# Kernel tuning notes

Hardware: AMD Instinct MI355X
Metric: run time of the kernel (lower is better)

The kernel has to match this reference:

```python
import jax, jax.numpy as jnp
import numpy as np

EPS_DIST = 1e-8
EPS_BN = 1e-5


def _bn_relu(x, g, b):
    # training-mode BatchNorm1d over (batch, spatial) per channel, then ReLU
    mean = jnp.mean(x, axis=(0, 2), keepdims=True)
    var = jnp.mean((x - mean) ** 2, axis=(0, 2), keepdims=True)
    xhat = (x - mean) * jax.lax.rsqrt(var + EPS_BN)
    return jax.nn.relu(xhat * g[None, :, None] + b[None, :, None])


def setup_inputs() -> dict:
    key = jax.random.key(0)
    ks = jax.random.split(key, 8)
    B, N, M, C1, C2 = 8, 16384, 4096, 64, 256
    return {
        "p1": jax.random.normal(ks[0], (B, N, 3), jnp.float32),
        "p2": jax.random.normal(ks[1], (B, M, 3), jnp.float32),
        "f1": jax.random.normal(ks[2], (B, C1, N), jnp.float32),
        "f2": jax.random.normal(ks[3], (B, C2, M), jnp.float32),
        "idx": jax.random.randint(ks[4], (B, N, 3), 0, M, jnp.int64),
        "W1": jax.random.normal(ks[5], (256, C1 + C2), jnp.float32) * 0.05,
        "g1": jnp.ones((256,), jnp.float32),
        "b1": jnp.zeros((256,), jnp.float32),
        "W2": jax.random.normal(ks[6], (256, 256), jnp.float32) * 0.05,
        "g2": jnp.ones((256,), jnp.float32),
        "b2": jnp.zeros((256,), jnp.float32),
    }


def reference(p1, p2, f1, f2, idx, W1, g1, b1, W2, g2, b2):
    B = p1.shape[0]
    b_ix = jnp.arange(B)[:, None, None]  # batch index for gathers
    # --- three_interpolation: inverse-squared-distance weighted 3-NN interp ---
    nbr_xyz = p2[b_ix, idx]                     # [B, N, 3, 3]
    d2 = jnp.sum((p1[:, :, None, :] - nbr_xyz) ** 2, axis=-1)  # [B, N, 3]
    recip = 1.0 / (d2 + EPS_DIST)
    weight = recip / jnp.sum(recip, axis=-1, keepdims=True)    # [B, N, 3]
    f2_nbr = jnp.swapaxes(f2, 1, 2)[b_ix, idx]  # [B, N, 3, C2]
    interp = jnp.einsum("bnkc,bnk->bcn", f2_nbr, weight)       # [B, C2, N]
    # --- concat + two 1x1 conv + BN + ReLU blocks ---
    x = jnp.concatenate((f1, interp), axis=1)   # [B, C1+C2, N]
    x = _bn_relu(jnp.einsum("oi,bin->bon", W1, x), g1, b1)
    x = _bn_relu(jnp.einsum("oi,bin->bon", W2, x), g2, b2)
    return x
```

## Files before the change

kernel.cpp:

```cpp
#include <hip/hip_runtime.h>
#include <hip/hip_bf16.h>

#define BB 8
#define NN 16384
#define MM 4096
#define C1 64
#define C2 256
#define K1 320
#define CO 256
#define MTOT (BB * NN)

#define STATS_OFF 0
#define FLAG_OFF  8192
#define W1B_OFF   16384
#define W2B_OFF   180224
#define F2T_OFF   327680
#define XT_OFF    (327680 + 16777216)
#define H2_OFF    (327680 + 16777216 + 83886080)

typedef short v8s __attribute__((ext_vector_type(8)));
typedef float v4f __attribute__((ext_vector_type(4)));

__device__ __forceinline__ float bf2f(unsigned short u) {
    unsigned v = ((unsigned)u) << 16;
    float f;
    __builtin_memcpy(&f, &v, 4);
    return f;
}
__device__ __forceinline__ unsigned short f2bf(float f) {
    unsigned u;
    __builtin_memcpy(&u, &f, 4);
    unsigned r = u + 0x7fffu + ((u >> 16) & 1u);
    return (unsigned short)(r >> 16);
}
__device__ __forceinline__ void gload16(const unsigned short* g, unsigned short* l) {
    __builtin_amdgcn_global_load_lds((const __attribute__((address_space(1))) unsigned int*)g,
                                     (__attribute__((address_space(3))) unsigned int*)l, 16, 0, 0);
}

__global__ void k_prep(const void* idx_raw, int* flag64, float* stats,
                       const float* __restrict__ W1, unsigned short* __restrict__ W1b,
                       const float* __restrict__ W2, unsigned short* __restrict__ W2b) {
    int blk = blockIdx.x;
    int t = threadIdx.x;
    if (blk < 320) {
        int e = blk * 256 + t;
        W1b[e] = f2bf(W1[e]);
    } else if (blk < 576) {
        int e = (blk - 320) * 256 + t;
        W2b[e] = f2bf(W2[e]);
    } else {
        for (int i = t; i < 8 * 256; i += 256) stats[i] = 0.f;
        if (t == 0) {
            const int* a = (const int*)idx_raw;
            int all0 = 1;
            for (int j = 1; j < 64; j += 2) all0 &= (a[j] == 0);
            *flag64 = all0;
        }
    }
}

__global__ void k_tr_f2(const float* __restrict__ f2, unsigned short* __restrict__ f2t) {
    __shared__ float tile[64][33];
    int b = blockIdx.z;
    int c0 = blockIdx.y * 64;
    int m0 = blockIdx.x * 32;
    int t = threadIdx.x;
    int lm = t & 31, lc = t >> 5;
    const float* src = f2 + ((size_t)b * C2 + c0) * MM + m0;
#pragma unroll
    for (int j = 0; j < 8; ++j)
        tile[lc + 8 * j][lm] = src[(size_t)(lc + 8 * j) * MM + lm];
    __syncthreads();
    int m = t >> 3, c8 = (t & 7) * 8;
    unsigned short tmp[8];
#pragma unroll
    for (int k = 0; k < 8; ++k) tmp[k] = f2bf(tile[c8 + k][m]);
    uint4 v;
    v.x = (unsigned)tmp[0] | ((unsigned)tmp[1] << 16);
    v.y = (unsigned)tmp[2] | ((unsigned)tmp[3] << 16);
    v.z = (unsigned)tmp[4] | ((unsigned)tmp[5] << 16);
    v.w = (unsigned)tmp[6] | ((unsigned)tmp[7] << 16);
    *(uint4*)&f2t[((size_t)b * MM + m0 + m) * C2 + c0 + c8] = v;
}

__global__ void k_tr_f1(const float* __restrict__ f1, unsigned short* __restrict__ xT) {
    __shared__ float tile[64][33];
    int b = blockIdx.z;
    int n0 = blockIdx.x * 32;
    int t = threadIdx.x;
    int lm = t & 31, lc = t >> 5;
    const float* src = f1 + ((size_t)b * C1) * NN + n0;
#pragma unroll
    for (int j = 0; j < 8; ++j)
        tile[lc + 8 * j][lm] = src[(size_t)(lc + 8 * j) * NN + lm];
    __syncthreads();
    int m = t >> 3, c8 = (t & 7) * 8;
    unsigned short tmp[8];
#pragma unroll
    for (int k = 0; k < 8; ++k) tmp[k] = f2bf(tile[c8 + k][m]);
    uint4 v;
    v.x = (unsigned)tmp[0] | ((unsigned)tmp[1] << 16);
    v.y = (unsigned)tmp[2] | ((unsigned)tmp[3] << 16);
    v.z = (unsigned)tmp[4] | ((unsigned)tmp[5] << 16);
    v.w = (unsigned)tmp[6] | ((unsigned)tmp[7] << 16);
    *(uint4*)&xT[((size_t)b * NN + n0 + m) * K1 + c8] = v;
}

__global__ void k_interp(const float* __restrict__ p1, const float* __restrict__ p2,
                         const void* __restrict__ idxv, const int* __restrict__ flag64,
                         const unsigned short* __restrict__ f2t,
                         unsigned short* __restrict__ xT) {
    int t = threadIdx.x;
    int p = t >> 5, lane = t & 31;
    size_t pt = (size_t)blockIdx.x * 8 + p;
    int b = (int)(pt >> 14);
    int m0, m1, m2;
    if (*flag64) {
        const long long* id = (const long long*)idxv;
        m0 = (int)id[pt * 3 + 0]; m1 = (int)id[pt * 3 + 1]; m2 = (int)id[pt * 3 + 2];
    } else {
        const int* id = (const int*)idxv;
        m0 = id[pt * 3 + 0]; m1 = id[pt * 3 + 1]; m2 = id[pt * 3 + 2];
    }
    float qx = p1[pt * 3 + 0], qy = p1[pt * 3 + 1], qz = p1[pt * 3 + 2];
    const float* pb = p2 + (size_t)b * MM * 3;
    float dx, dy, dz;
    dx = qx - pb[m0 * 3 + 0]; dy = qy - pb[m0 * 3 + 1]; dz = qz - pb[m0 * 3 + 2];
    float d0 = dx * dx + dy * dy + dz * dz;
    dx = qx - pb[m1 * 3 + 0]; dy = qy - pb[m1 * 3 + 1]; dz = qz - pb[m1 * 3 + 2];
    float d1 = dx * dx + dy * dy + dz * dz;
    dx = qx - pb[m2 * 3 + 0]; dy = qy - pb[m2 * 3 + 1]; dz = qz - pb[m2 * 3 + 2];
    float d2v = dx * dx + dy * dy + dz * dz;
    float r0 = 1.f / (d0 + 1e-8f), r1 = 1.f / (d1 + 1e-8f), r2 = 1.f / (d2v + 1e-8f);
    float inv = 1.f / (r0 + r1 + r2);
    float w0 = r0 * inv, w1 = r1 * inv, w2 = r2 * inv;

    const unsigned short* fb = f2t + (size_t)b * MM * C2;
    int c0 = lane * 8;
    uint4 va = *(const uint4*)(fb + (size_t)m0 * C2 + c0);
    uint4 vb = *(const uint4*)(fb + (size_t)m1 * C2 + c0);
    uint4 vc = *(const uint4*)(fb + (size_t)m2 * C2 + c0);

    float r[8];
    {
        const unsigned av[4] = {va.x, va.y, va.z, va.w};
        const unsigned bv[4] = {vb.x, vb.y, vb.z, vb.w};
        const unsigned cv[4] = {vc.x, vc.y, vc.z, vc.w};
#pragma unroll
        for (int q = 0; q < 4; ++q) {
            r[2 * q + 0] = w0 * bf2f((unsigned short)(av[q] & 0xffff))
                         + w1 * bf2f((unsigned short)(bv[q] & 0xffff))
                         + w2 * bf2f((unsigned short)(cv[q] & 0xffff));
            r[2 * q + 1] = w0 * bf2f((unsigned short)(av[q] >> 16))
                         + w1 * bf2f((unsigned short)(bv[q] >> 16))
                         + w2 * bf2f((unsigned short)(cv[q] >> 16));
        }
    }
    uint4 outv;
    outv.x = (unsigned)f2bf(r[0]) | ((unsigned)f2bf(r[1]) << 16);
    outv.y = (unsigned)f2bf(r[2]) | ((unsigned)f2bf(r[3]) << 16);
    outv.z = (unsigned)f2bf(r[4]) | ((unsigned)f2bf(r[5]) << 16);
    outv.w = (unsigned)f2bf(r[6]) | ((unsigned)f2bf(r[7]) << 16);
    *(uint4*)(xT + pt * K1 + C1 + c0) = outv;
}

#define TM 128
#define TN 128
#define TK 64
__launch_bounds__(256)
__global__ void k_gemm1(const unsigned short* __restrict__ xT,
                        const unsigned short* __restrict__ W1b,
                        unsigned short* __restrict__ h1,
                        float* __restrict__ sum1, float* __restrict__ ssq1) {
    __shared__ unsigned short smem[TM * TK + TN * TK];
    __shared__ float s_sum[TN], s_ssq[TN];
    unsigned short* As = smem;
    unsigned short* Bs = smem + TM * TK;
    const int t = threadIdx.x;
    const int lane = t & 63, w = t >> 6;
    const int wm = w >> 1, wc = w & 1;
    const long rbase = (long)blockIdx.x * TM;
    const int cb = blockIdx.y * TN;

    if (t < TN) { s_sum[t] = 0.f; s_ssq[t] = 0.f; }

    v4f acc[4][4];
#pragma unroll
    for (int r = 0; r < 4; ++r)
#pragma unroll
        for (int c = 0; c < 4; ++c) acc[r][c] = (v4f)(0.f);

    const int srow = w * 32 + (lane >> 3);
    const int sch = (lane & 7) * 8;
    const unsigned short* Ag = xT + (rbase + srow) * K1 + sch;
    const unsigned short* Bg = W1b + (size_t)(cb + srow) * K1 + sch;

    for (int k0 = 0; k0 < K1; k0 += TK) {
#pragma unroll
        for (int j = 0; j < 4; ++j) {
            gload16(Ag + (size_t)(j * 8) * K1 + k0, As + (w * 32 + j * 8) * TK);
            gload16(Bg + (size_t)(j * 8) * K1 + k0, Bs + (w * 32 + j * 8) * TK);
        }
        __syncthreads();
        const unsigned short* ApL = As + (wm * 64 + (lane & 15)) * TK + (lane >> 4) * 8;
        const unsigned short* BpL = Bs + (wc * 64 + (lane & 15)) * TK + (lane >> 4) * 8;
#pragma unroll
        for (int ks = 0; ks < 2; ++ks) {
            v8s af[4], bg[4];
#pragma unroll
            for (int r = 0; r < 4; ++r) af[r] = *(const v8s*)(ApL + r * 16 * TK + ks * 32);
#pragma unroll
            for (int c = 0; c < 4; ++c) bg[c] = *(const v8s*)(BpL + c * 16 * TK + ks * 32);
#pragma unroll
            for (int r = 0; r < 4; ++r)
#pragma unroll
                for (int c = 0; c < 4; ++c)
                    acc[r][c] = __builtin_amdgcn_mfma_f32_16x16x32_bf16(af[r], bg[c], acc[r][c], 0, 0, 0);
        }
        __syncthreads();
    }

    const int q = lane >> 4, ln = lane & 15;
#pragma unroll
    for (int c = 0; c < 4; ++c) {
        int col = wc * 64 + c * 16 + ln;
        int cc = col >> 3, ci = col & 7;
        float s = 0.f, sq = 0.f;
#pragma unroll
        for (int r = 0; r < 4; ++r)
#pragma unroll
            for (int i = 0; i < 4; ++i) {
                int row = wm * 64 + r * 16 + q * 4 + i;
                float v = acc[r][c][i];
                smem[row * 128 + 8 * (cc ^ (row & 15)) + ci] = f2bf(v);
                s += v; sq += v * v;
            }
        atomicAdd(&s_sum[col], s);
        atomicAdd(&s_ssq[col], sq);
    }
    __syncthreads();
    {
        int rr = t >> 4, cc2 = t & 15;
#pragma unroll
        for (int j = 0; j < 8; ++j) {
            int row = rr + 16 * j;
            uint4 v = *(const uint4*)&smem[row * 128 + 8 * (cc2 ^ (row & 15))];
            *(uint4*)&h1[(size_t)(rbase + row) * CO + cb + cc2 * 8] = v;
        }
    }
    if (t < TN) {
        atomicAdd(&sum1[cb + t], s_sum[t]);
        atomicAdd(&ssq1[cb + t], s_ssq[t]);
    }
}

__launch_bounds__(256)
__global__ void k_gemm2(const unsigned short* __restrict__ h1,
                        const unsigned short* __restrict__ W2b,
                        const float* __restrict__ sum1, const float* __restrict__ ssq1,
                        const float* __restrict__ g1, const float* __restrict__ b1,
                        unsigned short* __restrict__ h2,
                        float* __restrict__ sum2, float* __restrict__ ssq2) {
    __shared__ unsigned short smem[TM * TK + TN * TK];
    __shared__ float s_sum[TN], s_ssq[TN];
    __shared__ float sc1[CO], sh1[CO];
    unsigned short* As = smem;
    unsigned short* Bs = smem + TM * TK;
    const int t = threadIdx.x;
    const int lane = t & 63, w = t >> 6;
    const int wm = w >> 1, wc = w & 1;
    const long rbase = (long)blockIdx.x * TM;
    const int cb = blockIdx.y * TN;

    {
        const float invn = 1.f / (float)MTOT;
        float m = sum1[t] * invn;
        float v = ssq1[t] * invn - m * m;
        float s = g1[t] * rsqrtf(v + 1e-5f);
        sc1[t] = s;
        sh1[t] = b1[t] - m * s;
    }
    if (t < TN) { s_sum[t] = 0.f; s_ssq[t] = 0.f; }
    __syncthreads();

    v4f acc[4][4];
#pragma unroll
    for (int r = 0; r < 4; ++r)
#pragma unroll
        for (int c = 0; c < 4; ++c) acc[r][c] = (v4f)(0.f);

    const int srow = w * 32 + (lane >> 3);
    const int sch = (lane & 7) * 8;
    const unsigned short* Ag = h1 + (rbase + srow) * CO + sch;
    const unsigned short* Bg = W2b + (size_t)(cb + srow) * CO + sch;
    unsigned short* AsW = As + srow * TK + sch;

    for (int k0 = 0; k0 < CO; k0 += TK) {
#pragma unroll
        for (int j = 0; j < 4; ++j)
            gload16(Bg + (size_t)(j * 8) * CO + k0, Bs + (w * 32 + j * 8) * TK);
        float4 sca = *(const float4*)(sc1 + k0 + sch);
        float4 scb = *(const float4*)(sc1 + k0 + sch + 4);
        float4 sha = *(const float4*)(sh1 + k0 + sch);
        float4 shb = *(const float4*)(sh1 + k0 + sch + 4);
#pragma unroll
        for (int j = 0; j < 4; ++j) {
            uint4 av = *(const uint4*)(Ag + (size_t)(j * 8) * CO + k0);
            float y0 = fmaxf(bf2f((unsigned short)(av.x & 0xffff)) * sca.x + sha.x, 0.f);
            float y1 = fmaxf(bf2f((unsigned short)(av.x >> 16)) * sca.y + sha.y, 0.f);
            float y2 = fmaxf(bf2f((unsigned short)(av.y & 0xffff)) * sca.z + sha.z, 0.f);
            float y3 = fmaxf(bf2f((unsigned short)(av.y >> 16)) * sca.w + sha.w, 0.f);
            float y4 = fmaxf(bf2f((unsigned short)(av.z & 0xffff)) * scb.x + shb.x, 0.f);
            float y5 = fmaxf(bf2f((unsigned short)(av.z >> 16)) * scb.y + shb.y, 0.f);
            float y6 = fmaxf(bf2f((unsigned short)(av.w & 0xffff)) * scb.z + shb.z, 0.f);
            float y7 = fmaxf(bf2f((unsigned short)(av.w >> 16)) * scb.w + shb.w, 0.f);
            uint4 ov;
            ov.x = (unsigned)f2bf(y0) | ((unsigned)f2bf(y1) << 16);
            ov.y = (unsigned)f2bf(y2) | ((unsigned)f2bf(y3) << 16);
            ov.z = (unsigned)f2bf(y4) | ((unsigned)f2bf(y5) << 16);
            ov.w = (unsigned)f2bf(y6) | ((unsigned)f2bf(y7) << 16);
            *(uint4*)(AsW + (j * 8) * TK) = ov;
        }
        __syncthreads();
        const unsigned short* ApL = As + (wm * 64 + (lane & 15)) * TK + (lane >> 4) * 8;
        const unsigned short* BpL = Bs + (wc * 64 + (lane & 15)) * TK + (lane >> 4) * 8;
#pragma unroll
        for (int ks = 0; ks < 2; ++ks) {
            v8s af[4], bg4[4];
#pragma unroll
            for (int r = 0; r < 4; ++r) af[r] = *(const v8s*)(ApL + r * 16 * TK + ks * 32);
#pragma unroll
            for (int c = 0; c < 4; ++c) bg4[c] = *(const v8s*)(BpL + c * 16 * TK + ks * 32);
#pragma unroll
            for (int r = 0; r < 4; ++r)
#pragma unroll
                for (int c = 0; c < 4; ++c)
                    acc[r][c] = __builtin_amdgcn_mfma_f32_16x16x32_bf16(af[r], bg4[c], acc[r][c], 0, 0, 0);
        }
        __syncthreads();
    }

    const int q = lane >> 4, ln = lane & 15;
    const int b = (int)(rbase >> 14);
    const int nb = (int)(rbase & (NN - 1));
#pragma unroll
    for (int c = 0; c < 4; ++c) {
        int ol = wc * 64 + c * 16 + ln;
        float s = 0.f, sq = 0.f;
#pragma unroll
        for (int r = 0; r < 4; ++r)
#pragma unroll
            for (int i = 0; i < 4; ++i) {
                int row = wm * 64 + r * 16 + q * 4 + i;
                int rc = row >> 3, ri = row & 7;
                float v = acc[r][c][i];
                smem[ol * 128 + 8 * (rc ^ (ol & 15)) + ri] = f2bf(v);
                s += v; sq += v * v;
            }
        atomicAdd(&s_sum[ol], s);
        atomicAdd(&s_ssq[ol], sq);
    }
    __syncthreads();
    {
        int oo = t >> 4, nc = t & 15;
#pragma unroll
        for (int j = 0; j < 8; ++j) {
            int ol = oo + 16 * j;
            uint4 v = *(const uint4*)&smem[ol * 128 + 8 * (nc ^ (ol & 15))];
            *(uint4*)&h2[(((size_t)(b * CO + cb + ol)) << 14) + nb + nc * 8] = v;
        }
    }
    if (t < TN) {
        atomicAdd(&sum2[cb + t], s_sum[t]);
        atomicAdd(&ssq2[cb + t], s_ssq[t]);
    }
}

__global__ void k_apply(const unsigned short* __restrict__ h2,
                        const float* __restrict__ sum2, const float* __restrict__ ssq2,
                        const float* __restrict__ g2, const float* __restrict__ b2,
                        float* __restrict__ out) {
    __shared__ float ss[2];
    int o = (blockIdx.x >> 4) & 255;
    if (threadIdx.x == 0) {
        const float invn = 1.f / (float)MTOT;
        float m = sum2[o] * invn;
        float v = ssq2[o] * invn - m * m;
        float s = g2[o] * rsqrtf(v + 1e-5f);
        ss[0] = s;
        ss[1] = b2[o] - m * s;
    }
    __syncthreads();
    float s = ss[0], d = ss[1];
    size_t i = ((size_t)blockIdx.x * 256 + threadIdx.x) * 4;
    ushort4 hv = *(const ushort4*)(h2 + i);
    float4 v;
    v.x = fmaxf(bf2f(hv.x) * s + d, 0.f);
    v.y = fmaxf(bf2f(hv.y) * s + d, 0.f);
    v.z = fmaxf(bf2f(hv.z) * s + d, 0.f);
    v.w = fmaxf(bf2f(hv.w) * s + d, 0.f);
    *(float4*)&out[i] = v;
}

extern "C" void kernel_launch(void* const* d_in, const int* in_sizes, int n_in,
                              void* d_out, int out_size, void* d_ws, size_t ws_size,
                              hipStream_t stream) {
    const float* p1 = (const float*)d_in[0];
    const float* p2 = (const float*)d_in[1];
    const float* f1 = (const float*)d_in[2];
    const float* f2 = (const float*)d_in[3];
    const void*  idx = d_in[4];
    const float* W1 = (const float*)d_in[5];
    const float* g1 = (const float*)d_in[6];
    const float* b1 = (const float*)d_in[7];
    const float* W2 = (const float*)d_in[8];
    const float* g2 = (const float*)d_in[9];
    const float* b2 = (const float*)d_in[10];
    float* out = (float*)d_out;

    char* ws = (char*)d_ws;
    float* stats = (float*)(ws + STATS_OFF);
    float* sum1 = stats + 0;     float* ssq1 = stats + 256;
    float* sum2 = stats + 1024;  float* ssq2 = stats + 1280;
    int* flag64 = (int*)(ws + FLAG_OFF);
    unsigned short* W1b = (unsigned short*)(ws + W1B_OFF);
    unsigned short* W2b = (unsigned short*)(ws + W2B_OFF);
    unsigned short* f2t = (unsigned short*)(ws + F2T_OFF);
    unsigned short* xT  = (unsigned short*)(ws + XT_OFF);
    unsigned short* h2  = (unsigned short*)(ws + H2_OFF);

    unsigned short* h1 = (unsigned short*)d_out;

    k_prep<<<577, 256, 0, stream>>>(idx, flag64, stats, W1, W1b, W2, W2b);
    k_tr_f2<<<dim3(MM / 32, C2 / 64, BB), 256, 0, stream>>>(f2, f2t);
    k_tr_f1<<<dim3(NN / 32, 1, BB), 256, 0, stream>>>(f1, xT);
    k_interp<<<MTOT / 8, 256, 0, stream>>>(p1, p2, idx, flag64, f2t, xT);
    k_gemm1<<<dim3(MTOT / TM, CO / TN), 256, 0, stream>>>(xT, W1b, h1, sum1, ssq1);
    k_gemm2<<<dim3(MTOT / TM, CO / TN), 256, 0, stream>>>(h1, W2b, sum1, ssq1, g1, b1, h2, sum2, ssq2);
    k_apply<<<(int)((size_t)out_size / 4 / 256), 256, 0, stream>>>(h2, sum2, ssq2, g2, b2, out);
}
```

Baseline: 425.1 us.

## Double-buffer LDS tiles, swizzle layout, and write GEMM epilogues directly

Both GEMM kernels now use two LDS buffers so the next K-tile's global loads (and, in gemm2, the next activation register prefetch) are issued before the current tile's MFMAs, with manual waitcnt and barriers replacing __syncthreads. LDS rows get an XOR swizzle on the 16-byte chunk index to reduce bank conflicts, and gemm1 swaps operand roles so outputs come out transposed. The epilogues drop the LDS staging and block-level shared atomics: each wave writes packed bf16 pairs straight to global memory and reduces BN statistics with lane shuffles before issuing global atomics. In exchange, LDS use doubles, which may lower occupancy. The direct stores are narrower, 8-byte writes, so coalescing may suffer.

```diff
diff --git a/kernel.cpp b/kernel.cpp
--- a/kernel.cpp
+++ b/kernel.cpp
@@ -173,18 +173,14 @@
                         const unsigned short* __restrict__ W1b,
                         unsigned short* __restrict__ h1,
                         float* __restrict__ sum1, float* __restrict__ ssq1) {
-    __shared__ unsigned short smem[TM * TK + TN * TK];
-    __shared__ float s_sum[TN], s_ssq[TN];
-    unsigned short* As = smem;
-    unsigned short* Bs = smem + TM * TK;
+    __shared__ unsigned short smem[2][TM * TK + TN * TK];
     const int t = threadIdx.x;
     const int lane = t & 63, w = t >> 6;
-    const int wm = w >> 1, wc = w & 1;
+    const int cosub = (w >> 1) * 64;
+    const int nsub = (w & 1) * 64;
     const long rbase = (long)blockIdx.x * TM;
     const int cb = blockIdx.y * TN;
 
-    if (t < TN) { s_sum[t] = 0.f; s_ssq[t] = 0.f; }
-
     v4f acc[4][4];
 #pragma unroll
     for (int r = 0; r < 4; ++r)
@@ -192,66 +188,90 @@
         for (int c = 0; c < 4; ++c) acc[r][c] = (v4f)(0.f);
 
     const int srow = w * 32 + (lane >> 3);
-    const int sch = (lane & 7) * 8;
+    const int sch = ((lane & 7) ^ ((lane >> 3) & 7)) * 8;
     const unsigned short* Ag = xT + (rbase + srow) * K1 + sch;
     const unsigned short* Bg = W1b + (size_t)(cb + srow) * K1 + sch;
 
+#pragma unroll
+    for (int j = 0; j < 4; ++j) {
+        gload16(Ag + (size_t)(j * 8) * K1, smem[0] + (w * 32 + j * 8) * TK);
+        gload16(Bg + (size_t)(j * 8) * K1, smem[0] + TM * TK + (w * 32 + j * 8) * TK);
+    }
+
+    const int ln = lane & 15, q = lane >> 4;
+    const int xr = (lane & 7) * 8;
+
+#pragma unroll
     for (int k0 = 0; k0 < K1; k0 += TK) {
-#pragma unroll
-        for (int j = 0; j < 4; ++j) {
-            gload16(Ag + (size_t)(j * 8) * K1 + k0, As + (w * 32 + j * 8) * TK);
-            gload16(Bg + (size_t)(j * 8) * K1 + k0, Bs + (w * 32 + j * 8) * TK);
-        }
-        __syncthreads();
-        const unsigned short* ApL = As + (wm * 64 + (lane & 15)) * TK + (lane >> 4) * 8;
-        const unsigned short* BpL = Bs + (wc * 64 + (lane & 15)) * TK + (lane >> 4) * 8;
+        const int p = (k0 >> 6) & 1;
+        if (k0 + TK < K1) {
+#pragma unroll
+            for (int j = 0; j < 4; ++j) {
+                gload16(Ag + (size_t)(j * 8) * K1 + k0 + TK, smem[p ^ 1] + (w * 32 + j * 8) * TK);
+                gload16(Bg + (size_t)(j * 8) * K1 + k0 + TK, smem[p ^ 1] + TM * TK + (w * 32 + j * 8) * TK);
+            }
+            asm volatile("s_waitcnt vmcnt(8)" ::: "memory");
+        } else {
+            asm volatile("s_waitcnt vmcnt(0)" ::: "memory");
+        }
+        asm volatile("s_barrier" ::: "memory");
+        const unsigned short* Xs = smem[p];
+        const unsigned short* Ws = smem[p] + TM * TK;
 #pragma unroll
         for (int ks = 0; ks < 2; ++ks) {
-            v8s af[4], bg[4];
-#pragma unroll
-            for (int r = 0; r < 4; ++r) af[r] = *(const v8s*)(ApL + r * 16 * TK + ks * 32);
-#pragma unroll
-            for (int c = 0; c < 4; ++c) bg[c] = *(const v8s*)(BpL + c * 16 * TK + ks * 32);
+            const int off = (q * 8 + ks * 32) ^ xr;
+            v8s af[4], bx[4];
+#pragma unroll
+            for (int r = 0; r < 4; ++r) af[r] = *(const v8s*)(Ws + (cosub + r * 16 + ln) * TK + off);
+#pragma unroll
+            for (int c = 0; c < 4; ++c) bx[c] = *(const v8s*)(Xs + (nsub + c * 16 + ln) * TK + off);
 #pragma unroll
             for (int r = 0; r < 4; ++r)
 #pragma unroll
                 for (int c = 0; c < 4; ++c)
-                    acc[r][c] = __builtin_amdgcn_mfma_f32_16x16x32_bf16(af[r], bg[c], acc[r][c], 0, 0, 0);
-        }
-        __syncthreads();
-    }
-
-    const int q = lane >> 4, ln = lane & 15;
-#pragma unroll
-    for (int c = 0; c < 4; ++c) {
-        int col = wc * 64 + c * 16 + ln;
-        int cc = col >> 3, ci = col & 7;
-        float s = 0.f, sq = 0.f;
+                    acc[r][c] = __builtin_amdgcn_mfma_f32_16x16x32_bf16(af[r], bx[c], acc[r][c], 0, 0, 0);
+        }
+        if (k0 + TK < K1) asm volatile("s_barrier" ::: "memory");
+    }
+
+    float s[4][4], sq[4][4];
+#pragma unroll
+    for (int r = 0; r < 4; ++r)
+#pragma unroll
+        for (int i = 0; i < 4; ++i) { s[r][i] = 0.f; sq[r][i] = 0.f; }
+#pragma unroll
+    for (int r = 0; r < 4; ++r) {
+#pragma unroll
+        for (int c = 0; c < 4; ++c) {
+            float v0 = acc[r][c][0], v1 = acc[r][c][1], v2 = acc[r][c][2], v3 = acc[r][c][3];
+            uint2 ov;
+            ov.x = (unsigned)f2bf(v0) | ((unsigned)f2bf(v1) << 16);
+            ov.y = (unsigned)f2bf(v2) | ((unsigned)f2bf(v3) << 16);
+            *(uint2*)&h1[(size_t)(rbase + nsub + c * 16 + ln) * CO + cb + cosub + r * 16 + q * 4] = ov;
+            s[r][0] += v0; sq[r][0] += v0 * v0;
+            s[r][1] += v1; sq[r][1] += v1 * v1;
+            s[r][2] += v2; sq[r][2] += v2 * v2;
+            s[r][3] += v3; sq[r][3] += v3 * v3;
+        }
+    }
+#pragma unroll
+    for (int m = 1; m <= 8; m <<= 1) {
 #pragma unroll
         for (int r = 0; r < 4; ++r)
 #pragma unroll
             for (int i = 0; i < 4; ++i) {
-                int row = wm * 64 + r * 16 + q * 4 + i;
-                float v = acc[r][c][i];
-                smem[row * 128 + 8 * (cc ^ (row & 15)) + ci] = f2bf(v);
-                s += v; sq += v * v;
+                s[r][i] += __shfl_xor(s[r][i], m);
+                sq[r][i] += __shfl_xor(sq[r][i], m);
             }
-        atomicAdd(&s_sum[col], s);
-        atomicAdd(&s_ssq[col], sq);
-    }
-    __syncthreads();
-    {
-        int rr = t >> 4, cc2 = t & 15;
-#pragma unroll
-        for (int j = 0; j < 8; ++j) {
-            int row = rr + 16 * j;
-            uint4 v = *(const uint4*)&smem[row * 128 + 8 * (cc2 ^ (row & 15))];
-            *(uint4*)&h1[(size_t)(rbase + row) * CO + cb + cc2 * 8] = v;
-        }
-    }
-    if (t < TN) {
-        atomicAdd(&sum1[cb + t], s_sum[t]);
-        atomicAdd(&ssq1[cb + t], s_ssq[t]);
+    }
+    if (ln == 0) {
+#pragma unroll
+        for (int r = 0; r < 4; ++r)
+#pragma unroll
+            for (int i = 0; i < 4; ++i) {
+                atomicAdd(&sum1[cb + cosub + r * 16 + q * 4 + i], s[r][i]);
+                atomicAdd(&ssq1[cb + cosub + r * 16 + q * 4 + i], sq[r][i]);
+            }
     }
 }
 
@@ -262,14 +282,12 @@
                         const float* __restrict__ g1, const float* __restrict__ b1,
                         unsigned short* __restrict__ h2,
                         float* __restrict__ sum2, float* __restrict__ ssq2) {
-    __shared__ unsigned short smem[TM * TK + TN * TK];
-    __shared__ float s_sum[TN], s_ssq[TN];
+    __shared__ unsigned short smem[2][TM * TK + TN * TK];
     __shared__ float sc1[CO], sh1[CO];
-    unsigned short* As = smem;
-    unsigned short* Bs = smem + TM * TK;
     const int t = threadIdx.x;
     const int lane = t & 63, w = t >> 6;
-    const int wm = w >> 1, wc = w & 1;
+    const int nsub = (w >> 1) * 64;
+    const int cosub = (w & 1) * 64;
     const long rbase = (long)blockIdx.x * TM;
     const int cb = blockIdx.y * TN;
 
@@ -277,11 +295,10 @@
         const float invn = 1.f / (float)MTOT;
         float m = sum1[t] * invn;
         float v = ssq1[t] * invn - m * m;
-        float s = g1[t] * rsqrtf(v + 1e-5f);
-        sc1[t] = s;
-        sh1[t] = b1[t] - m * s;
-    }
-    if (t < TN) { s_sum[t] = 0.f; s_ssq[t] = 0.f; }
+        float sgl = g1[t] * rsqrtf(v + 1e-5f);
+        sc1[t] = sgl;
+        sh1[t] = b1[t] - m * sgl;
+    }
     __syncthreads();
 
     v4f acc[4][4];
@@ -291,89 +308,110 @@
         for (int c = 0; c < 4; ++c) acc[r][c] = (v4f)(0.f);
 
     const int srow = w * 32 + (lane >> 3);
-    const int sch = (lane & 7) * 8;
-    const unsigned short* Ag = h1 + (rbase + srow) * CO + sch;
+    const int schl = (lane & 7) * 8;
+    const int sch = ((lane & 7) ^ ((lane >> 3) & 7)) * 8;
+    const unsigned short* Ag = h1 + (rbase + srow) * CO + schl;
     const unsigned short* Bg = W2b + (size_t)(cb + srow) * CO + sch;
-    unsigned short* AsW = As + srow * TK + sch;
-
+
+    uint4 avc[4];
+#pragma unroll
+    for (int j = 0; j < 4; ++j) avc[j] = *(const uint4*)(Ag + (size_t)(j * 8) * CO);
+#pragma unroll
+    for (int j = 0; j < 4; ++j)
+        gload16(Bg + (size_t)(j * 8) * CO, smem[0] + TM * TK + (w * 32 + j * 8) * TK);
+
+    const int ln = lane & 15, q = lane >> 4;
+    const int xr = (lane & 7) * 8;
+
+#pragma unroll
     for (int k0 = 0; k0 < CO; k0 += TK) {
-#pragma unroll
-        for (int j = 0; j < 4; ++j)
-            gload16(Bg + (size_t)(j * 8) * CO + k0, Bs + (w * 32 + j * 8) * TK);
-        float4 sca = *(const float4*)(sc1 + k0 + sch);
-        float4 scb = *(const float4*)(sc1 + k0 + sch + 4);
-        float4 sha = *(const float4*)(sh1 + k0 + sch);
-        float4 shb = *(const float4*)(sh1 + k0 + sch + 4);
-#pragma unroll
-        for (int j = 0; j < 4; ++j) {
-            uint4 av = *(const uint4*)(Ag + (size_t)(j * 8) * CO + k0);
-            float y0 = fmaxf(bf2f((unsigned short)(av.x & 0xffff)) * sca.x + sha.x, 0.f);
-            float y1 = fmaxf(bf2f((unsigned short)(av.x >> 16)) * sca.y + sha.y, 0.f);
-            float y2 = fmaxf(bf2f((unsigned short)(av.y & 0xffff)) * sca.z + sha.z, 0.f);
-            float y3 = fmaxf(bf2f((unsigned short)(av.y >> 16)) * sca.w + sha.w, 0.f);
-            float y4 = fmaxf(bf2f((unsigned short)(av.z & 0xffff)) * scb.x + shb.x, 0.f);
-            float y5 = fmaxf(bf2f((unsigned short)(av.z >> 16)) * scb.y + shb.y, 0.f);
-            float y6 = fmaxf(bf2f((unsigned short)(av.w & 0xffff)) * scb.z + shb.z, 0.f);
-            float y7 = fmaxf(bf2f((unsigned short)(av.w >> 16)) * scb.w + shb.w, 0.f);
-            uint4 ov;
-            ov.x = (unsigned)f2bf(y0) | ((unsigned)f2bf(y1) << 16);
-            ov.y = (unsigned)f2bf(y2) | ((unsigned)f2bf(y3) << 16);
-            ov.z = (unsigned)f2bf(y4) | ((unsigned)f2bf(y5) << 16);
-            ov.w = (unsigned)f2bf(y6) | ((unsigned)f2bf(y7) << 16);
-            *(uint4*)(AsW + (j * 8) * TK) = ov;
-        }
-        __syncthreads();
-        const unsigned short* ApL = As + (wm * 64 + (lane & 15)) * TK + (lane >> 4) * 8;
-        const unsigned short* BpL = Bs + (wc * 64 + (lane & 15)) * TK + (lane >> 4) * 8;
+        const int p = (k0 >> 6) & 1;
+        const bool notlast = (k0 + TK < CO);
+        uint4 avn[4];
+        if (notlast) {
+#pragma unroll
+            for (int j = 0; j < 4; ++j)
+                avn[j] = *(const uint4*)(Ag + (size_t)(j * 8) * CO + k0 + TK);
+        }
+        {
+            float4 sca = *(const float4*)(sc1 + k0 + schl);
+            float4 scb = *(const float4*)(sc1 + k0 + schl + 4);
+            float4 sha = *(const float4*)(sh1 + k0 + schl);
+            float4 shb = *(const float4*)(sh1 + k0 + schl + 4);
+            unsigned short* dst = smem[p] + srow * TK + sch;
+#pragma unroll
+            for (int j = 0; j < 4; ++j) {
+                uint4 av = avc[j];
+                float y0 = fmaxf(bf2f((unsigned short)(av.x & 0xffff)) * sca.x + sha.x, 0.f);
+                float y1 = fmaxf(bf2f((unsigned short)(av.x >> 16)) * sca.y + sha.y, 0.f);
+                float y2 = fmaxf(bf2f((unsigned short)(av.y & 0xffff)) * sca.z + sha.z, 0.f);
+                float y3 = fmaxf(bf2f((unsigned short)(av.y >> 16)) * sca.w + sha.w, 0.f);
+                float y4 = fmaxf(bf2f((unsigned short)(av.z & 0xffff)) * scb.x + shb.x, 0.f);
+                float y5 = fmaxf(bf2f((unsigned short)(av.z >> 16)) * scb.y + shb.y, 0.f);
+                float y6 = fmaxf(bf2f((unsigned short)(av.w & 0xffff)) * scb.z + shb.z, 0.f);
+                float y7 = fmaxf(bf2f((unsigned short)(av.w >> 16)) * scb.w + shb.w, 0.f);
+                uint4 ov;
+                ov.x = (unsigned)f2bf(y0) | ((unsigned)f2bf(y1) << 16);
+                ov.y = (unsigned)f2bf(y2) | ((unsigned)f2bf(y3) << 16);
+                ov.z = (unsigned)f2bf(y4) | ((unsigned)f2bf(y5) << 16);
+                ov.w = (unsigned)f2bf(y6) | ((unsigned)f2bf(y7) << 16);
+                *(uint4*)(dst + (j * 8) * TK) = ov;
+            }
+        }
+        if (notlast) {
+#pragma unroll
+            for (int j = 0; j < 4; ++j)
+                gload16(Bg + (size_t)(j * 8) * CO + k0 + TK, smem[p ^ 1] + TM * TK + (w * 32 + j * 8) * TK);
+            asm volatile("s_waitcnt vmcnt(8)" ::: "memory");
+        } else {
+            asm volatile("s_waitcnt vmcnt(0)" ::: "memory");
+        }
+        asm volatile("s_waitcnt lgkmcnt(0)" ::: "memory");
+        asm volatile("s_barrier" ::: "memory");
+        const unsigned short* As = smem[p];
+        const unsigned short* Ws = smem[p] + TM * TK;
 #pragma unroll
         for (int ks = 0; ks < 2; ++ks) {
-            v8s af[4], bg4[4];
-#pragma unroll
-            for (int r = 0; r < 4; ++r) af[r] = *(const v8s*)(ApL + r * 16 * TK + ks * 32);
-#pragma unroll
-            for (int c = 0; c < 4; ++c) bg4[c] = *(const v8s*)(BpL + c * 16 * TK + ks * 32);
+            const int off = (q * 8 + ks * 32) ^ xr;
+            v8s af[4], bw[4];
+#pragma unroll
+            for (int r = 0; r < 4; ++r) af[r] = *(const v8s*)(As + (nsub + r * 16 + ln) * TK + off);
+#pragma unroll
+            for (int c = 0; c < 4; ++c) bw[c] = *(const v8s*)(Ws + (cosub + c * 16 + ln) * TK + off);
 #pragma unroll
             for (int r = 0; r < 4; ++r)
 #pragma unroll
                 for (int c = 0; c < 4; ++c)
-                    acc[r][c] = __builtin_amdgcn_mfma_f32_16x16x32_bf16(af[r], bg4[c], acc[r][c], 0, 0, 0);
-        }
-        __syncthreads();
-    }
-
-    const int q = lane >> 4, ln = lane & 15;
+                    acc[r][c] = __builtin_amdgcn_mfma_f32_16x16x32_bf16(af[r], bw[c], acc[r][c], 0, 0, 0);
+        }
+        if (notlast) {
+            asm volatile("s_barrier" ::: "memory");
+#pragma unroll
+            for (int j = 0; j < 4; ++j) avc[j] = avn[j];
+        }
+    }
+
     const int b = (int)(rbase >> 14);
     const int nb = (int)(rbase & (NN - 1));
 #pragma unroll
     for (int c = 0; c < 4; ++c) {
-        int ol = wc * 64 + c * 16 + ln;
         float s = 0.f, sq = 0.f;
 #pragma unroll
-        for (int r = 0; r < 4; ++r)
-#pragma unroll
-            for (int i = 0; i < 4; ++i) {
-                int row = wm * 64 + r * 16 + q * 4 + i;
-                int rc = row >> 3, ri = row & 7;
-                float v = acc[r][c][i];
-                smem[ol * 128 + 8 * (rc ^ (ol & 15)) + ri] = f2bf(v);
-                s += v; sq += v * v;
-            }
-        atomicAdd(&s_sum[ol], s);
-        atomicAdd(&s_ssq[ol], sq);
-    }
-    __syncthreads();
-    {
-        int oo = t >> 4, nc = t & 15;
-#pragma unroll
-        for (int j = 0; j < 8; ++j) {
-            int ol = oo + 16 * j;
-            uint4 v = *(const uint4*)&smem[ol * 128 + 8 * (nc ^ (ol & 15))];
-            *(uint4*)&h2[(((size_t)(b * CO + cb + ol)) << 14) + nb + nc * 8] = v;
-        }
-    }
-    if (t < TN) {
-        atomicAdd(&sum2[cb + t], s_sum[t]);
-        atomicAdd(&ssq2[cb + t], s_ssq[t]);
+        for (int r = 0; r < 4; ++r) {
+            float v0 = acc[r][c][0], v1 = acc[r][c][1], v2 = acc[r][c][2], v3 = acc[r][c][3];
+            uint2 ov;
+            ov.x = (unsigned)f2bf(v0) | ((unsigned)f2bf(v1) << 16);
+            ov.y = (unsigned)f2bf(v2) | ((unsigned)f2bf(v3) << 16);
+            *(uint2*)&h2[(((size_t)(b * CO + cb + cosub + c * 16 + ln)) << 14) + nb + nsub + r * 16 + q * 4] = ov;
+            s += v0 + v1 + v2 + v3;
+            sq += v0 * v0 + v1 * v1 + v2 * v2 + v3 * v3;
+        }
+        s += __shfl_xor(s, 16); sq += __shfl_xor(sq, 16);
+        s += __shfl_xor(s, 32); sq += __shfl_xor(sq, 32);
+        if (lane < 16) {
+            atomicAdd(&sum2[cb + cosub + c * 16 + lane], s);
+            atomicAdd(&ssq2[cb + cosub + c * 16 + lane], sq);
+        }
     }
 }
 
```

Result: slower. 688.1 us (+61.9%).

## XOR-swizzle GEMM operand layouts to avoid LDS bank conflicts

Applied to the files above, without the earlier changes.

Producers of xT, W1b and W2b now store each row's 8-element chunks at a column XORed with (row&7)*8. The GEMM kernels read LDS fragments with the matching XOR offset, and gemm2's activation writes into As use the same swizzle. The goal is to remove LDS bank conflicts on the strided 64-element rows read by the MFMA fragment loads, since global_load_lds copies the pre-swizzled global layout straight into shared memory. The risk is that every producer and consumer must agree on the swizzle, and any unseen consumer of xT or W would read permuted data.

```diff
diff --git a/kernel.cpp b/kernel.cpp
--- a/kernel.cpp
+++ b/kernel.cpp
@@ -18,6 +18,7 @@
 #define XT_OFF    (327680 + 16777216)
 #define H2_OFF    (327680 + 16777216 + 83886080)
 
+
 typedef short v8s __attribute__((ext_vector_type(8)));
 typedef float v4f __attribute__((ext_vector_type(4)));
 
@@ -45,10 +46,12 @@
     int t = threadIdx.x;
     if (blk < 320) {
         int e = blk * 256 + t;
-        W1b[e] = f2bf(W1[e]);
+        int row = e / K1, col = e - row * K1;
+        W1b[row * K1 + (col ^ ((row & 7) << 3))] = f2bf(W1[e]);
     } else if (blk < 576) {
         int e = (blk - 320) * 256 + t;
-        W2b[e] = f2bf(W2[e]);
+        int row = e >> 8, col = e & 255;
+        W2b[row * CO + (col ^ ((row & 7) << 3))] = f2bf(W2[e]);
     } else {
         for (int i = t; i < 8 * 256; i += 256) stats[i] = 0.f;
         if (t == 0) {
@@ -104,7 +107,7 @@
     v.y = (unsigned)tmp[2] | ((unsigned)tmp[3] << 16);
     v.z = (unsigned)tmp[4] | ((unsigned)tmp[5] << 16);
     v.w = (unsigned)tmp[6] | ((unsigned)tmp[7] << 16);
-    *(uint4*)&xT[((size_t)b * NN + n0 + m) * K1 + c8] = v;
+    *(uint4*)&xT[((size_t)b * NN + n0 + m) * K1 + (c8 ^ ((m & 7) * 8))] = v;
 }
 
 __global__ void k_interp(const float* __restrict__ p1, const float* __restrict__ p2,
@@ -162,7 +165,7 @@
     outv.y = (unsigned)f2bf(r[2]) | ((unsigned)f2bf(r[3]) << 16);
     outv.z = (unsigned)f2bf(r[4]) | ((unsigned)f2bf(r[5]) << 16);
     outv.w = (unsigned)f2bf(r[6]) | ((unsigned)f2bf(r[7]) << 16);
-    *(uint4*)(xT + pt * K1 + C1 + c0) = outv;
+    *(uint4*)(xT + pt * K1 + ((C1 + c0) ^ (((int)pt & 7) * 8))) = outv;
 }
 
 #define TM 128
@@ -196,6 +199,9 @@
     const unsigned short* Ag = xT + (rbase + srow) * K1 + sch;
     const unsigned short* Bg = W1b + (size_t)(cb + srow) * K1 + sch;
 
+    const int ln = lane & 15, q = lane >> 4;
+    const int xs = (ln & 7) * 8;
+
     for (int k0 = 0; k0 < K1; k0 += TK) {
 #pragma unroll
         for (int j = 0; j < 4; ++j) {
@@ -203,15 +209,16 @@
             gload16(Bg + (size_t)(j * 8) * K1 + k0, Bs + (w * 32 + j * 8) * TK);
         }
         __syncthreads();
-        const unsigned short* ApL = As + (wm * 64 + (lane & 15)) * TK + (lane >> 4) * 8;
-        const unsigned short* BpL = Bs + (wc * 64 + (lane & 15)) * TK + (lane >> 4) * 8;
+        const unsigned short* ApL = As + (wm * 64 + ln) * TK;
+        const unsigned short* BpL = Bs + (wc * 64 + ln) * TK;
 #pragma unroll
         for (int ks = 0; ks < 2; ++ks) {
+            const int off = (q * 8 + ks * 32) ^ xs;
             v8s af[4], bg[4];
 #pragma unroll
-            for (int r = 0; r < 4; ++r) af[r] = *(const v8s*)(ApL + r * 16 * TK + ks * 32);
-#pragma unroll
-            for (int c = 0; c < 4; ++c) bg[c] = *(const v8s*)(BpL + c * 16 * TK + ks * 32);
+            for (int r = 0; r < 4; ++r) af[r] = *(const v8s*)(ApL + r * 16 * TK + off);
+#pragma unroll
+            for (int c = 0; c < 4; ++c) bg[c] = *(const v8s*)(BpL + c * 16 * TK + off);
 #pragma unroll
             for (int r = 0; r < 4; ++r)
 #pragma unroll
@@ -221,7 +228,6 @@
         __syncthreads();
     }
 
-    const int q = lane >> 4, ln = lane & 15;
 #pragma unroll
     for (int c = 0; c < 4; ++c) {
         int col = wc * 64 + c * 16 + ln;
@@ -294,7 +300,7 @@
     const int sch = (lane & 7) * 8;
     const unsigned short* Ag = h1 + (rbase + srow) * CO + sch;
     const unsigned short* Bg = W2b + (size_t)(cb + srow) * CO + sch;
-    unsigned short* AsW = As + srow * TK + sch;
+    unsigned short* AsW = As + srow * TK + (sch ^ ((srow & 7) * 8));
 
     for (int k0 = 0; k0 < CO; k0 += TK) {
 #pragma unroll
@@ -323,15 +329,18 @@
             *(uint4*)(AsW + (j * 8) * TK) = ov;
         }
         __syncthreads();
-        const unsigned short* ApL = As + (wm * 64 + (lane & 15)) * TK + (lane >> 4) * 8;
-        const unsigned short* BpL = Bs + (wc * 64 + (lane & 15)) * TK + (lane >> 4) * 8;
+        const int ln = lane & 15, q = lane >> 4;
+        const int xs = (ln & 7) * 8;
+        const unsigned short* ApL = As + (wm * 64 + ln) * TK;
+        const unsigned short* BpL = Bs + (wc * 64 + ln) * TK;
 #pragma unroll
         for (int ks = 0; ks < 2; ++ks) {
+            const int off = (q * 8 + ks * 32) ^ xs;
             v8s af[4], bg4[4];
 #pragma unroll
-            for (int r = 0; r < 4; ++r) af[r] = *(const v8s*)(ApL + r * 16 * TK + ks * 32);
-#pragma unroll
-            for (int c = 0; c < 4; ++c) bg4[c] = *(const v8s*)(BpL + c * 16 * TK + ks * 32);
+            for (int r = 0; r < 4; ++r) af[r] = *(const v8s*)(ApL + r * 16 * TK + off);
+#pragma unroll
+            for (int c = 0; c < 4; ++c) bg4[c] = *(const v8s*)(BpL + c * 16 * TK + off);
 #pragma unroll
             for (int r = 0; r < 4; ++r)
 #pragma unroll
```

Measured after the change: 423.1 us. Within noise of the previous version (-0.5%).
